# Kernel tuning notes

Measured on AMD Instinct MI355X. Metric: run time of the kernel, lower is better.

Reference implementation:

```python
import jax, jax.numpy as jnp
import numpy as np

CHEB_K = 3

def avwgcn(x, E, W_pool, b_pool):
    # x: [B,N,Cin], E: [N,e], W_pool: [e,K,Cin,Cout], b_pool: [e,Cout]
    N = E.shape[0]
    A = jax.nn.softmax(jax.nn.relu(E @ E.T), axis=1)          # adaptive adjacency [N,N]
    supports = [jnp.eye(N, dtype=x.dtype), A]
    for _ in range(2, CHEB_K):
        supports.append(2.0 * (A @ supports[-1]) - supports[-2])
    S = jnp.stack(supports)                                    # [K,N,N]
    W = jnp.einsum('ne,ekio->nkio', E, W_pool)                 # per-node weights
    b = E @ b_pool                                             # [N,Cout]
    xg = jnp.einsum('knm,bmi->bnki', S, x)                     # Chebyshev graph conv
    return jnp.einsum('bnki,nkio->bno', xg, W) + b


def setup_inputs() -> dict:
    key = jax.random.key(0)
    ks = jax.random.split(key, 7)
    B, N, Din, Dout, E_DIM = 64, 1024, 64, 64, 16
    C = Din + Dout
    return {
        'x': jax.random.normal(ks[0], (B, N, Din), dtype=jnp.float32),
        'state': jax.random.normal(ks[1], (B, N, Dout), dtype=jnp.float32),
        'node_embeddings': jax.random.normal(ks[2], (N, E_DIM), dtype=jnp.float32),
        'gate_W_pool': jax.random.normal(ks[3], (E_DIM, CHEB_K, C, 2 * Dout), dtype=jnp.float32) * 0.1,
        'gate_b_pool': jax.random.normal(ks[4], (E_DIM, 2 * Dout), dtype=jnp.float32) * 0.1,
        'upd_W_pool': jax.random.normal(ks[5], (E_DIM, CHEB_K, C, Dout), dtype=jnp.float32) * 0.1,
        'upd_b_pool': jax.random.normal(ks[6], (E_DIM, Dout), dtype=jnp.float32) * 0.1,
    }


def reference(x, state, node_embeddings, gate_W_pool, gate_b_pool, upd_W_pool, upd_b_pool):
    hidden_dim = state.shape[-1]
    input_and_state = jnp.concatenate([x, state], axis=-1)
    z_r = jax.nn.sigmoid(avwgcn(input_and_state, node_embeddings, gate_W_pool, gate_b_pool))
    z, r = z_r[..., :hidden_dim], z_r[..., hidden_dim:]
    candidate = jnp.concatenate([x, z * state], axis=-1)
    hc = jnp.tanh(avwgcn(candidate, node_embeddings, upd_W_pool, upd_b_pool))
    return r * state + (1.0 - r) * hc
```

## Files before the change

### kernel.cpp

```cpp
#include <hip/hip_runtime.h>
#include <math.h>

#define N_NODES 1024
#define B_SZ 64
#define GNH 4096
#define KI 384
#define EDIM 16

typedef _Float16 half8_t __attribute__((ext_vector_type(8)));
typedef float f32x4 __attribute__((ext_vector_type(4)));

__device__ __forceinline__ unsigned short f2h(float f) {
    _Float16 h = (_Float16)f;
    return *(unsigned short*)&h;
}
__device__ __forceinline__ float h2f(unsigned short u) {
    _Float16 h = *(_Float16*)&u;
    return (float)h;
}
__device__ __forceinline__ float sigmoidf_(float v) {
    return 1.f / (1.f + __expf(-v));
}
__device__ __forceinline__ void load_lds16(const void* g, void* l) {
    __builtin_amdgcn_global_load_lds(
        (const __attribute__((address_space(1))) void*)g,
        (__attribute__((address_space(3))) void*)l, 16, 0, 0);
}

__global__ __launch_bounds__(256) void compute_A_kernel(
    const float* __restrict__ E, unsigned short* __restrict__ Ah) {
    __shared__ float red[256];
    const int tid = threadIdx.x;
    const int n = blockIdx.x;
    float en[EDIM];
#pragma unroll
    for (int e = 0; e < EDIM; ++e) en[e] = E[n * EDIM + e];
    float logit[4], lmax = -1e30f;
#pragma unroll
    for (int j = 0; j < 4; ++j) {
        const int m = tid + j * 256;
        float d = 0.f;
#pragma unroll
        for (int e = 0; e < EDIM; ++e) d += en[e] * E[m * EDIM + e];
        d = fmaxf(d, 0.f);
        logit[j] = d;
        lmax = fmaxf(lmax, d);
    }
    red[tid] = lmax;
    __syncthreads();
    for (int s = 128; s > 0; s >>= 1) {
        if (tid < s) red[tid] = fmaxf(red[tid], red[tid + s]);
        __syncthreads();
    }
    lmax = red[0];
    __syncthreads();
    float ex[4], lsum = 0.f;
#pragma unroll
    for (int j = 0; j < 4; ++j) {
        ex[j] = __expf(logit[j] - lmax);
        lsum += ex[j];
    }
    red[tid] = lsum;
    __syncthreads();
    for (int s = 128; s > 0; s >>= 1) {
        if (tid < s) red[tid] += red[tid + s];
        __syncthreads();
    }
    const float inv = 1.f / red[0];
#pragma unroll
    for (int j = 0; j < 4; ++j)
        Ah[n * N_NODES + tid + j * 256] = f2h(ex[j] * inv);
}

__global__ __launch_bounds__(256) void build_T0_all_kernel(
    const float* __restrict__ x, const float* __restrict__ state,
    unsigned short* __restrict__ TX0, unsigned short* __restrict__ TS0,
    unsigned short* __restrict__ TX0T, unsigned short* __restrict__ TS0T) {
    __shared__ unsigned short Lx[64 * 72];
    __shared__ unsigned short Lss[64 * 72];
    const int tid = threadIdx.x;
    const int n0 = blockIdx.x * 64;
    const int b = blockIdx.y;
#pragma unroll
    for (int t = 0; t < 16; ++t) {
        const int id = t * 256 + tid;
        const int nl = id >> 6;
        const int c = id & 63;
        const float xv = x[((size_t)b * N_NODES + n0 + nl) * 64 + c];
        const float sv = state[((size_t)b * N_NODES + n0 + nl) * 64 + c];
        const unsigned short xh = f2h(xv), sh = f2h(sv);
        TX0[(size_t)(n0 + nl) * GNH + b * 64 + c] = xh;
        TS0[(size_t)(n0 + nl) * GNH + b * 64 + c] = sh;
        Lx[c * 72 + nl] = xh;
        Lss[c * 72 + nl] = sh;
    }
    __syncthreads();
#pragma unroll
    for (int t = 0; t < 2; ++t) {
        const int id = t * 256 + tid;
        const int c = id >> 3;
        const int n8 = id & 7;
        uint4 xv = *(const uint4*)&Lx[c * 72 + n8 * 8];
        uint4 sv = *(const uint4*)&Lss[c * 72 + n8 * 8];
        *(uint4*)&TX0T[(size_t)(b * 64 + c) * N_NODES + n0 + n8 * 8] = xv;
        *(uint4*)&TS0T[(size_t)(b * 64 + c) * N_NODES + n0 + n8 * 8] = sv;
    }
}

__global__ __launch_bounds__(256) void transpose16_kernel(
    const unsigned short* __restrict__ src, unsigned short* __restrict__ dst,
    int W) {
    __shared__ unsigned short Ls[64 * 72];
    const int tid = threadIdx.x;
    const int r0 = blockIdx.x * 64;
    const int c0 = blockIdx.y * 64;
#pragma unroll
    for (int t = 0; t < 2; ++t) {
        const int id = t * 256 + tid;
        const int row = id >> 3;
        const int c8 = id & 7;
        uint4 v = *(const uint4*)&src[(size_t)(r0 + row) * W + c0 + c8 * 8];
        const unsigned short* vp = (const unsigned short*)&v;
#pragma unroll
        for (int j = 0; j < 8; ++j) Ls[(c8 * 8 + j) * 72 + row] = vp[j];
    }
    __syncthreads();
#pragma unroll
    for (int t = 0; t < 2; ++t) {
        const int id = t * 256 + tid;
        const int c = id >> 3;
        const int r8 = id & 7;
        uint4 v = *(const uint4*)&Ls[c * 72 + r8 * 8];
        *(uint4*)&dst[(size_t)(c0 + c) * N_NODES + r0 + r8 * 8] = v;
    }
}

__global__ __launch_bounds__(256) void gemm_s2_kernel(
    const unsigned short* __restrict__ Ah,
    const unsigned short* __restrict__ AhT, unsigned short* __restrict__ S2h) {
    __shared__ unsigned short As[64 * 64];
    __shared__ unsigned short Bs[64 * 64];
    const int tid = threadIdx.x;
    const int wave = tid >> 6;
    const int lane = tid & 63;
    const int l15 = lane & 15;
    const int quad = lane >> 4;
    const int n0 = blockIdx.x * 64;
    const int m0 = blockIdx.y * 64;
    const int wn = wave * 16;
    const int lr = lane >> 3;
    const int lsw = (lane & 7) ^ lr;

    f32x4 acc[4] = {};
    for (int k0 = 0; k0 < N_NODES; k0 += 64) {
#pragma unroll
        for (int i = 0; i < 2; ++i) {
            const int rbase = (wave * 2 + i) * 8;
            load_lds16(&Ah[(size_t)(n0 + rbase + lr) * N_NODES + k0 + lsw * 8],
                       &As[rbase * 64]);
            load_lds16(&AhT[(size_t)(m0 + rbase + lr) * N_NODES + k0 + lsw * 8],
                       &Bs[rbase * 64]);
        }
        __syncthreads();
#pragma unroll
        for (int ks = 0; ks < 2; ++ks) {
            const int slot = ((ks * 4 + quad) ^ (l15 & 7)) * 8;
            const half8_t b = *(const half8_t*)&Bs[(wn + l15) * 64 + slot];
#pragma unroll
            for (int mi = 0; mi < 4; ++mi) {
                const half8_t a = *(const half8_t*)&As[(mi * 16 + l15) * 64 + slot];
                acc[mi] =
                    __builtin_amdgcn_mfma_f32_16x16x32_f16(a, b, acc[mi], 0, 0, 0);
            }
        }
        __syncthreads();
    }
#pragma unroll
    for (int mi = 0; mi < 4; ++mi) {
#pragma unroll
        for (int r = 0; r < 4; ++r) {
            const int n_g = n0 + mi * 16 + quad * 4 + r;
            const int m_g = m0 + wn + l15;
            const float v = 2.f * acc[mi][r] - (n_g == m_g ? 1.f : 0.f);
            S2h[(size_t)n_g * N_NODES + m_g] = f2h(v);
        }
    }
}

template <int BM>
__global__ __launch_bounds__(512, 2) void gemm_graph8_kernel(
    const unsigned short* __restrict__ Ah,
    const unsigned short* __restrict__ S2h,
    const unsigned short* __restrict__ BTX,
    const unsigned short* __restrict__ BTS,
    unsigned short* __restrict__ T1X, unsigned short* __restrict__ T1S,
    unsigned short* __restrict__ T2X, unsigned short* __restrict__ T2S,
    int ysplit, int colsPerXcd) {
    constexpr int MFR = BM / 32;
    constexpr int ASLOT_H = BM * 32;
    constexpr int SLOT_H = ASLOT_H + 8192;
    constexpr int APASS = BM / 128;
    constexpr int MT = 2048 / BM;
    __shared__ unsigned short lds[4 * SLOT_H];

    const int tid = threadIdx.x;
    const int wave = tid >> 6;
    const int lane = tid & 63;
    const int l15 = lane & 15;
    const int quad = lane >> 4;
    const int wm = (wave >> 2) * (BM / 2);
    const int wn = (wave & 3) * 64;

    const int id = blockIdx.x;
    const int xcd = id & 7;
    const int j = id >> 3;
    const int mtile = j & (MT - 1);
    const int ytile = xcd * colsPerXcd + j / MT;
    const int mrow0 = mtile * BM;
    const bool isA = mrow0 < N_NODES;
    const unsigned short* Asrc =
        (isA ? Ah : S2h) + (size_t)(mrow0 & 1023) * N_NODES;
    const bool isX = ytile < ysplit;
    const int col0 = (isX ? ytile : ytile - ysplit) * 256;
    const unsigned short* Bsrc = (isX ? BTX : BTS) + (size_t)col0 * N_NODES;
    unsigned short* OUT = (isA ? (isX ? T1X : T1S) : (isX ? T2X : T2S)) +
                          (size_t)(mrow0 & 1023) * GNH + col0;

    int goff[2];
#pragma unroll
    for (int jp = 0; jp < 2; ++jp) {
        const int cell = jp * 512 + tid;
        const int prow = cell >> 3;
        const int q = (cell & 7) ^ (prow & 7);
        goff[jp] = (2 * prow + (q >> 2)) * N_NODES + (q & 3) * 8;
    }

    int offA[MFR], offB[4];
#pragma unroll
    for (int mi = 0; mi < MFR; ++mi) {
        const int prow = (wm >> 1) + mi * 8 + (l15 >> 1);
        const int s8 = ((l15 & 1) * 4 + quad) ^ (prow & 7);
        offA[mi] = prow * 64 + s8 * 8;
    }
#pragma unroll
    for (int ni = 0; ni < 4; ++ni) {
        const int pcol = (wn >> 1) + ni * 8 + (l15 >> 1);
        const int s8 = ((l15 & 1) * 4 + quad) ^ (pcol & 7);
        offB[ni] = ASLOT_H + pcol * 64 + s8 * 8;
    }

    f32x4 acc[MFR][4] = {};

    auto stageA = [&](int t) {
        const int sl = t & 3;
#pragma unroll
        for (int jp = 0; jp < APASS; ++jp)
            load_lds16(Asrc + (size_t)t * 32 + goff[jp],
                       &lds[sl * SLOT_H + jp * 4096 + wave * 512]);
    };
    auto stageB = [&](int t) {
        const int sl = t & 3;
#pragma unroll
        for (int jp = 0; jp < 2; ++jp)
            load_lds16(Bsrc + (size_t)t * 32 + goff[jp],
                       &lds[sl * SLOT_H + ASLOT_H + jp * 4096 + wave * 512]);
    };
    auto waitPipe = [&] {
        if constexpr (BM == 256)
            asm volatile("s_waitcnt vmcnt(8)" ::: "memory");
        else
            asm volatile("s_waitcnt vmcnt(6)" ::: "memory");
    };

    auto tileBody = [&](int t, bool tail) {
        const unsigned short* base = &lds[(t & 3) * SLOT_H];
        half8_t a[MFR], b0, b1, b2, b3;
#pragma unroll
        for (int mi = 0; mi < MFR; ++mi)
            a[mi] = *(const half8_t*)&base[offA[mi]];
        b0 = *(const half8_t*)&base[offB[0]];
        b1 = *(const half8_t*)&base[offB[1]];
        if (!tail) stageA(t + 3);
        __builtin_amdgcn_sched_barrier(0);
        __builtin_amdgcn_s_barrier();
        asm volatile("s_waitcnt lgkmcnt(0)" ::: "memory");
        __builtin_amdgcn_sched_barrier(0);
        __builtin_amdgcn_s_setprio(1);
#pragma unroll
        for (int mi = 0; mi < MFR; ++mi) {
            acc[mi][0] = __builtin_amdgcn_mfma_f32_16x16x32_f16(
                a[mi], b0, acc[mi][0], 0, 0, 0);
            acc[mi][1] = __builtin_amdgcn_mfma_f32_16x16x32_f16(
                a[mi], b1, acc[mi][1], 0, 0, 0);
        }
        __builtin_amdgcn_s_setprio(0);
        __builtin_amdgcn_sched_barrier(0);
        __builtin_amdgcn_s_barrier();
        b2 = *(const half8_t*)&base[offB[2]];
        b3 = *(const half8_t*)&base[offB[3]];
        if (!tail) {
            stageB(t + 3);
            waitPipe();
        } else {
            asm volatile("s_waitcnt vmcnt(0)" ::: "memory");
        }
        __builtin_amdgcn_sched_barrier(0);
        __builtin_amdgcn_s_barrier();
        asm volatile("s_waitcnt lgkmcnt(0)" ::: "memory");
        __builtin_amdgcn_sched_barrier(0);
        __builtin_amdgcn_s_setprio(1);
#pragma unroll
        for (int mi = 0; mi < MFR; ++mi) {
            acc[mi][2] = __builtin_amdgcn_mfma_f32_16x16x32_f16(
                a[mi], b2, acc[mi][2], 0, 0, 0);
            acc[mi][3] = __builtin_amdgcn_mfma_f32_16x16x32_f16(
                a[mi], b3, acc[mi][3], 0, 0, 0);
        }
        __builtin_amdgcn_s_setprio(0);
        __builtin_amdgcn_sched_barrier(0);
        __builtin_amdgcn_s_barrier();
    };

    stageA(0); stageB(0);
    stageA(1); stageB(1);
    stageA(2); stageB(2);
    waitPipe();
    __builtin_amdgcn_s_barrier();
    __builtin_amdgcn_sched_barrier(0);

#pragma unroll 4
    for (int t = 0; t < 28; ++t) tileBody(t, false);
    tileBody(28, false);
    tileBody(29, true);
    tileBody(30, true);
    tileBody(31, true);

    constexpr int NPASS = BM / 64;
#pragma unroll
    for (int p = 0; p < NPASS; ++p) {
        __syncthreads();
        const int whalf = (BM == 256) ? (p >> 1) : p;
        const int mi0 = (BM == 256) ? (p & 1) * 4 : 0;
        if ((wave >> 2) == whalf) {
#pragma unroll
            for (int mi = 0; mi < 4; ++mi)
#pragma unroll
                for (int ni = 0; ni < 4; ++ni)
#pragma unroll
                    for (int r = 0; r < 4; ++r) {
                        const int row = mi * 16 + quad * 4 + r;
                        const int col = wn + ni * 16 + l15;
                        lds[row * 264 + col] = f2h(acc[mi0 + mi][ni][r]);
                    }
        }
        __syncthreads();
#pragma unroll
        for (int i = 0; i < 4; ++i) {
            const int id2 = i * 512 + tid;
            const int row = id2 >> 5;
            const int c8 = id2 & 31;
            uint4 v = *(const uint4*)&lds[row * 264 + c8 * 8];
            *(uint4*)&OUT[(size_t)(p * 64 + row) * GNH + c8 * 8] = v;
        }
    }
}

__global__ __launch_bounds__(256) void dequant_kernel(
    const float* __restrict__ Wp, const float* __restrict__ E,
    unsigned short* __restrict__ Wt, int NO) {
    __shared__ float En[32 * 16];
    const int tid = threadIdx.x;
    const int ki0 = blockIdx.x * 32;
    const int o0 = blockIdx.y * 32;
    const int n0 = blockIdx.z * 32;
    const int o = tid >> 3;
    const int k4 = tid & 7;

#pragma unroll
    for (int t = 0; t < 2; ++t) {
        const int id = t * 256 + tid;
        En[id] = E[(n0 + (id >> 4)) * EDIM + (id & 15)];
    }
    __syncthreads();

    f32x4 w[EDIM];
#pragma unroll
    for (int e = 0; e < EDIM; ++e) {
        f32x4 v;
#pragma unroll
        for (int j = 0; j < 4; ++j)
            v[j] = Wp[(size_t)(e * KI + ki0 + k4 * 4 + j) * NO + o0 + o];
        w[e] = v;
    }

    const size_t wt_base = ((size_t)n0 * NO + (o0 + o)) * KI + ki0 + k4 * 4;
#pragma unroll 4
    for (int nl = 0; nl < 32; ++nl) {
        f32x4 a = {0.f, 0.f, 0.f, 0.f};
#pragma unroll
        for (int e = 0; e < EDIM; ++e) a += w[e] * En[nl * EDIM + e];
        union { unsigned short u[4]; uint2 v; } pk;
#pragma unroll
        for (int j = 0; j < 4; ++j) pk.u[j] = f2h(a[j]);
        *(uint2*)&Wt[wt_base + (size_t)nl * NO * KI] = pk.v;
    }
}

__global__ __launch_bounds__(256) void pernode_gate_kernel(
    const unsigned short* __restrict__ TX0,
    const unsigned short* __restrict__ TS0,
    const unsigned short* __restrict__ TX1,
    const unsigned short* __restrict__ TS1,
    const unsigned short* __restrict__ TX2,
    const unsigned short* __restrict__ TS2,
    const unsigned short* __restrict__ Wt, const float* __restrict__ E,
    const float* __restrict__ bp, const float* __restrict__ state,
    unsigned short* __restrict__ rbuf, unsigned short* __restrict__ ts0_out) {
    __shared__ unsigned short XsX[64 * 64];
    __shared__ unsigned short XsS[64 * 64];
    const int n = blockIdx.x;
    const int tid = threadIdx.x;
    const int wave = tid >> 6;
    const int lane = tid & 63;
    const int l15 = lane & 15;
    const int quad = lane >> 4;
    const int wn = wave * 32;
    const int lr = lane >> 3;
    const int lsw = (lane & 7) ^ lr;

    float bias[2];
#pragma unroll
    for (int ni = 0; ni < 2; ++ni) {
        float bv = 0.f;
#pragma unroll
        for (int e = 0; e < EDIM; ++e)
            bv += E[n * EDIM + e] * bp[e * 128 + wn + ni * 16 + l15];
        bias[ni] = bv;
    }

    f32x4 acc[4][2] = {};

    const unsigned short* TXs[3] = {TX0, TX1, TX2};
    const unsigned short* TSs[3] = {TS0, TS1, TS2};
    const unsigned short* wrow0 = Wt + ((size_t)n * 128 + wn + l15) * KI;
    const unsigned short* wrow1 = Wt + ((size_t)n * 128 + wn + 16 + l15) * KI;

    for (int s = 0; s < 3; ++s) {
        const unsigned short* xs = TXs[s] + (size_t)n * GNH;
        const unsigned short* ss = TSs[s] + (size_t)n * GNH;
#pragma unroll
        for (int i = 0; i < 2; ++i) {
            const int slab = wave * 2 + i;
            load_lds16(xs + (slab * 8 + lr) * 64 + lsw * 8, &XsX[slab * 512]);
            load_lds16(ss + (slab * 8 + lr) * 64 + lsw * 8, &XsS[slab * 512]);
        }
        __syncthreads();
#pragma unroll
        for (int ks = 0; ks < 4; ++ks) {
            const int kseg = ks * 4 + quad;
            half8_t b[2];
            b[0] = *(const half8_t*)&wrow0[s * 128 + kseg * 8];
            b[1] = *(const half8_t*)&wrow1[s * 128 + kseg * 8];
            const unsigned short* plane = (kseg < 8) ? XsX : XsS;
            const int aslot = ((kseg & 7) ^ (l15 & 7)) * 8;
#pragma unroll
            for (int mi = 0; mi < 4; ++mi) {
                const half8_t a =
                    *(const half8_t*)&plane[(mi * 16 + l15) * 64 + aslot];
#pragma unroll
                for (int ni = 0; ni < 2; ++ni)
                    acc[mi][ni] = __builtin_amdgcn_mfma_f32_16x16x32_f16(
                        a, b[ni], acc[mi][ni], 0, 0, 0);
            }
        }
        __syncthreads();
    }

#pragma unroll
    for (int mi = 0; mi < 4; ++mi) {
#pragma unroll
        for (int r = 0; r < 4; ++r) {
            const int b_g = mi * 16 + quad * 4 + r;
#pragma unroll
            for (int ni = 0; ni < 2; ++ni) {
                const int o_g = wn + ni * 16 + l15;
                const float v = sigmoidf_(acc[mi][ni][r] + bias[ni]);
                if (o_g < 64) {
                    const float sv =
                        state[((size_t)b_g * N_NODES + n) * 64 + o_g];
                    ts0_out[(size_t)n * GNH + b_g * 64 + o_g] = f2h(v * sv);
                } else {
                    rbuf[((size_t)n * B_SZ + b_g) * 64 + (o_g - 64)] = f2h(v);
                }
            }
        }
    }
}

__global__ __launch_bounds__(256) void pernode_upd_kernel(
    const unsigned short* __restrict__ TX0,
    const unsigned short* __restrict__ TS0,
    const unsigned short* __restrict__ TX1,
    const unsigned short* __restrict__ TS1,
    const unsigned short* __restrict__ TX2,
    const unsigned short* __restrict__ TS2,
    const unsigned short* __restrict__ Wt, const float* __restrict__ E,
    const float* __restrict__ bp, const float* __restrict__ state,
    const unsigned short* __restrict__ rbuf, float* __restrict__ out) {
    __shared__ unsigned short XsX[64 * 64];
    __shared__ unsigned short XsS[64 * 64];
    const int n = blockIdx.x;
    const int tid = threadIdx.x;
    const int wave = tid >> 6;
    const int lane = tid & 63;
    const int l15 = lane & 15;
    const int quad = lane >> 4;
    const int wn = wave * 16;
    const int o_g = wn + l15;
    const int lr = lane >> 3;
    const int lsw = (lane & 7) ^ lr;

    float bias = 0.f;
#pragma unroll
    for (int e = 0; e < EDIM; ++e)
        bias += E[n * EDIM + e] * bp[e * 64 + o_g];

    f32x4 acc[4] = {};

    const unsigned short* TXs[3] = {TX0, TX1, TX2};
    const unsigned short* TSs[3] = {TS0, TS1, TS2};
    const unsigned short* wrow = Wt + ((size_t)n * 64 + o_g) * KI;

    for (int s = 0; s < 3; ++s) {
        const unsigned short* xs = TXs[s] + (size_t)n * GNH;
        const unsigned short* ss = TSs[s] + (size_t)n * GNH;
#pragma unroll
        for (int i = 0; i < 2; ++i) {
            const int slab = wave * 2 + i;
            load_lds16(xs + (slab * 8 + lr) * 64 + lsw * 8, &XsX[slab * 512]);
            load_lds16(ss + (slab * 8 + lr) * 64 + lsw * 8, &XsS[slab * 512]);
        }
        __syncthreads();
#pragma unroll
        for (int ks = 0; ks < 4; ++ks) {
            const int kseg = ks * 4 + quad;
            const half8_t b = *(const half8_t*)&wrow[s * 128 + kseg * 8];
            const unsigned short* plane = (kseg < 8) ? XsX : XsS;
            const int aslot = ((kseg & 7) ^ (l15 & 7)) * 8;
#pragma unroll
            for (int mi = 0; mi < 4; ++mi) {
                const half8_t a =
                    *(const half8_t*)&plane[(mi * 16 + l15) * 64 + aslot];
                acc[mi] = __builtin_amdgcn_mfma_f32_16x16x32_f16(a, b, acc[mi],
                                                                 0, 0, 0);
            }
        }
        __syncthreads();
    }

#pragma unroll
    for (int mi = 0; mi < 4; ++mi) {
#pragma unroll
        for (int r = 0; r < 4; ++r) {
            const int b_g = mi * 16 + quad * 4 + r;
            const float hc = tanhf(acc[mi][r] + bias);
            const float rr = h2f(rbuf[((size_t)n * B_SZ + b_g) * 64 + o_g]);
            const float sv = state[((size_t)b_g * N_NODES + n) * 64 + o_g];
            out[((size_t)b_g * N_NODES + n) * 64 + o_g] =
                rr * sv + (1.f - rr) * hc;
        }
    }
}

extern "C" void kernel_launch(void* const* d_in, const int* in_sizes, int n_in,
                              void* d_out, int out_size, void* d_ws,
                              size_t ws_size, hipStream_t stream) {
    const float* x = (const float*)d_in[0];
    const float* state = (const float*)d_in[1];
    const float* E = (const float*)d_in[2];
    const float* gW = (const float*)d_in[3];
    const float* gb = (const float*)d_in[4];
    const float* uW = (const float*)d_in[5];
    const float* ub = (const float*)d_in[6];
    float* out = (float*)d_out;

    char* ws = (char*)d_ws;
    unsigned short* Ah = (unsigned short*)ws;
    unsigned short* AhT = (unsigned short*)(ws + 2097152);
    unsigned short* S2h = (unsigned short*)(ws + 4194304);
    unsigned short* TX0 = (unsigned short*)(ws + 6291456);
    unsigned short* TS0 = (unsigned short*)(ws + 14680064);
    unsigned short* TX0T = (unsigned short*)(ws + 23068672);
    unsigned short* TS0T = (unsigned short*)(ws + 31457280);
    unsigned short* TX1 = (unsigned short*)(ws + 39845888);
    unsigned short* TS1 = (unsigned short*)(ws + 48234496);
    unsigned short* TX2 = (unsigned short*)(ws + 56623104);
    unsigned short* TS2 = (unsigned short*)(ws + 65011712);
    unsigned short* Wt = (unsigned short*)(ws + 73400320);
    unsigned short* rbuf = (unsigned short*)(ws + 174063616);

    compute_A_kernel<<<N_NODES, 256, 0, stream>>>(E, Ah);
    build_T0_all_kernel<<<dim3(16, 64), 256, 0, stream>>>(x, state, TX0, TS0,
                                                          TX0T, TS0T);
    transpose16_kernel<<<dim3(16, 16), 256, 0, stream>>>(Ah, AhT, N_NODES);
    gemm_s2_kernel<<<dim3(16, 16), 256, 0, stream>>>(Ah, AhT, S2h);

    gemm_graph8_kernel<256><<<256, 512, 0, stream>>>(
        Ah, S2h, TX0T, TS0T, TX1, TS1, TX2, TS2, 16, 4);
    dequant_kernel<<<dim3(12, 4, 32), 256, 0, stream>>>(gW, E, Wt, 128);
    pernode_gate_kernel<<<N_NODES, 256, 0, stream>>>(
        TX0, TS0, TX1, TS1, TX2, TS2, Wt, E, gb, state, rbuf, TS0);
    transpose16_kernel<<<dim3(16, 64), 256, 0, stream>>>(TS0, TS0T, GNH);

    gemm_graph8_kernel<128><<<256, 512, 0, stream>>>(
        Ah, S2h, TX0T, TS0T, TX1, TS1, TX2, TS2, 0, 2);
    dequant_kernel<<<dim3(12, 2, 32), 256, 0, stream>>>(uW, E, Wt, 64);
    pernode_upd_kernel<<<N_NODES, 256, 0, stream>>>(
        TX0, TS0, TX1, TS1, TX2, TS2, Wt, E, ub, state, rbuf, out);
}
```

Measured before the change: 293.2 us.

## Double-buffer LDS stages and preload weights in per-node gate/update kernels

The per-node gate and update kernels now load all weight fragments into registers up front. They double-buffer the three Chebyshev stages in LDS, issuing loads for the next stage while MFMAs run on the current one, with explicit vmcnt waits and barriers in place of the loop's syncthreads. The gate output now goes to a separate CAND buffer instead of overwriting TS0 in place, which avoids a write-after-read hazard now that stages are prefetched. The cost is more register pressure from the preloaded weights, twice the LDS, and hand-tuned wait counts that must match the issued loads.

Result: no change. 291.8 us (-0.5%).

```diff
diff --git a/kernel.cpp b/kernel.cpp
--- a/kernel.cpp
+++ b/kernel.cpp
@@ -25,6 +25,9 @@
     __builtin_amdgcn_global_load_lds(
         (const __attribute__((address_space(1))) void*)g,
         (__attribute__((address_space(3))) void*)l, 16, 0, 0);
+}
+__device__ __forceinline__ void fence_sched() {
+    __builtin_amdgcn_sched_barrier(0);
 }
 
 __global__ __launch_bounds__(256) void compute_A_kernel(
@@ -415,9 +418,8 @@
     const unsigned short* __restrict__ TS2,
     const unsigned short* __restrict__ Wt, const float* __restrict__ E,
     const float* __restrict__ bp, const float* __restrict__ state,
-    unsigned short* __restrict__ rbuf, unsigned short* __restrict__ ts0_out) {
-    __shared__ unsigned short XsX[64 * 64];
-    __shared__ unsigned short XsS[64 * 64];
+    unsigned short* __restrict__ rbuf, unsigned short* __restrict__ cand) {
+    __shared__ unsigned short Xs[2][2][4096];
     const int n = blockIdx.x;
     const int tid = threadIdx.x;
     const int wave = tid >> 6;
@@ -428,6 +430,16 @@
     const int lr = lane >> 3;
     const int lsw = (lane & 7) ^ lr;
 
+    const unsigned short* wrow0 = Wt + ((size_t)n * 128 + wn + l15) * KI;
+    const unsigned short* wrow1 = Wt + ((size_t)n * 128 + wn + 16 + l15) * KI;
+    half8_t wf[3][4][2];
+#pragma unroll
+    for (int s = 0; s < 3; ++s)
+#pragma unroll
+        for (int ks = 0; ks < 4; ++ks) {
+            wf[s][ks][0] = *(const half8_t*)&wrow0[s * 128 + (ks * 4 + quad) * 8];
+            wf[s][ks][1] = *(const half8_t*)&wrow1[s * 128 + (ks * 4 + quad) * 8];
+        }
     float bias[2];
 #pragma unroll
     for (int ni = 0; ni < 2; ++ni) {
@@ -438,30 +450,29 @@
         bias[ni] = bv;
     }
 
-    f32x4 acc[4][2] = {};
-
     const unsigned short* TXs[3] = {TX0, TX1, TX2};
     const unsigned short* TSs[3] = {TS0, TS1, TS2};
-    const unsigned short* wrow0 = Wt + ((size_t)n * 128 + wn + l15) * KI;
-    const unsigned short* wrow1 = Wt + ((size_t)n * 128 + wn + 16 + l15) * KI;
-
-    for (int s = 0; s < 3; ++s) {
+
+    auto STAGE = [&](int s, int bf) {
         const unsigned short* xs = TXs[s] + (size_t)n * GNH;
         const unsigned short* ss = TSs[s] + (size_t)n * GNH;
 #pragma unroll
         for (int i = 0; i < 2; ++i) {
             const int slab = wave * 2 + i;
-            load_lds16(xs + (slab * 8 + lr) * 64 + lsw * 8, &XsX[slab * 512]);
-            load_lds16(ss + (slab * 8 + lr) * 64 + lsw * 8, &XsS[slab * 512]);
-        }
-        __syncthreads();
+            load_lds16(xs + (slab * 8 + lr) * 64 + lsw * 8,
+                       &Xs[bf][0][slab * 512]);
+            load_lds16(ss + (slab * 8 + lr) * 64 + lsw * 8,
+                       &Xs[bf][1][slab * 512]);
+        }
+    };
+
+    f32x4 acc[4][2] = {};
+    auto MFMAS = [&](int s, int bf) {
 #pragma unroll
         for (int ks = 0; ks < 4; ++ks) {
             const int kseg = ks * 4 + quad;
-            half8_t b[2];
-            b[0] = *(const half8_t*)&wrow0[s * 128 + kseg * 8];
-            b[1] = *(const half8_t*)&wrow1[s * 128 + kseg * 8];
-            const unsigned short* plane = (kseg < 8) ? XsX : XsS;
+            const unsigned short* plane = (kseg < 8) ? &Xs[bf][0][0]
+                                                     : &Xs[bf][1][0];
             const int aslot = ((kseg & 7) ^ (l15 & 7)) * 8;
 #pragma unroll
             for (int mi = 0; mi < 4; ++mi) {
@@ -470,11 +481,34 @@
 #pragma unroll
                 for (int ni = 0; ni < 2; ++ni)
                     acc[mi][ni] = __builtin_amdgcn_mfma_f32_16x16x32_f16(
-                        a, b[ni], acc[mi][ni], 0, 0, 0);
+                        a, wf[s][ks][ni], acc[mi][ni], 0, 0, 0);
             }
         }
-        __syncthreads();
-    }
+    };
+
+    fence_sched();
+    asm volatile("s_waitcnt vmcnt(0)" ::: "memory");
+    fence_sched();
+    STAGE(0, 0);
+    STAGE(1, 1);
+    fence_sched();
+    asm volatile("s_waitcnt vmcnt(4)" ::: "memory");
+    fence_sched();
+    __builtin_amdgcn_s_barrier();
+    MFMAS(0, 0);
+    fence_sched();
+    __builtin_amdgcn_s_barrier();
+    STAGE(2, 0);
+    fence_sched();
+    asm volatile("s_waitcnt vmcnt(4)" ::: "memory");
+    fence_sched();
+    __builtin_amdgcn_s_barrier();
+    MFMAS(1, 1);
+    fence_sched();
+    asm volatile("s_waitcnt vmcnt(0)" ::: "memory");
+    fence_sched();
+    __builtin_amdgcn_s_barrier();
+    MFMAS(2, 0);
 
 #pragma unroll
     for (int mi = 0; mi < 4; ++mi) {
@@ -488,7 +522,7 @@
                 if (o_g < 64) {
                     const float sv =
                         state[((size_t)b_g * N_NODES + n) * 64 + o_g];
-                    ts0_out[(size_t)n * GNH + b_g * 64 + o_g] = f2h(v * sv);
+                    cand[(size_t)n * GNH + b_g * 64 + o_g] = f2h(v * sv);
                 } else {
                     rbuf[((size_t)n * B_SZ + b_g) * 64 + (o_g - 64)] = f2h(v);
                 }
@@ -499,7 +533,7 @@
 
 __global__ __launch_bounds__(256) void pernode_upd_kernel(
     const unsigned short* __restrict__ TX0,
-    const unsigned short* __restrict__ TS0,
+    const unsigned short* __restrict__ CAND,
     const unsigned short* __restrict__ TX1,
     const unsigned short* __restrict__ TS1,
     const unsigned short* __restrict__ TX2,
@@ -507,8 +541,7 @@
     const unsigned short* __restrict__ Wt, const float* __restrict__ E,
     const float* __restrict__ bp, const float* __restrict__ state,
     const unsigned short* __restrict__ rbuf, float* __restrict__ out) {
-    __shared__ unsigned short XsX[64 * 64];
-    __shared__ unsigned short XsS[64 * 64];
+    __shared__ unsigned short Xs[2][2][4096];
     const int n = blockIdx.x;
     const int tid = threadIdx.x;
     const int wave = tid >> 6;
@@ -520,43 +553,75 @@
     const int lr = lane >> 3;
     const int lsw = (lane & 7) ^ lr;
 
+    const unsigned short* wrow = Wt + ((size_t)n * 64 + o_g) * KI;
+    half8_t wf[3][4];
+#pragma unroll
+    for (int s = 0; s < 3; ++s)
+#pragma unroll
+        for (int ks = 0; ks < 4; ++ks)
+            wf[s][ks] = *(const half8_t*)&wrow[s * 128 + (ks * 4 + quad) * 8];
     float bias = 0.f;
 #pragma unroll
     for (int e = 0; e < EDIM; ++e)
         bias += E[n * EDIM + e] * bp[e * 64 + o_g];
 
-    f32x4 acc[4] = {};
-
     const unsigned short* TXs[3] = {TX0, TX1, TX2};
-    const unsigned short* TSs[3] = {TS0, TS1, TS2};
-    const unsigned short* wrow = Wt + ((size_t)n * 64 + o_g) * KI;
-
-    for (int s = 0; s < 3; ++s) {
+    const unsigned short* TSs[3] = {CAND, TS1, TS2};
+
+    auto STAGE = [&](int s, int bf) {
         const unsigned short* xs = TXs[s] + (size_t)n * GNH;
         const unsigned short* ss = TSs[s] + (size_t)n * GNH;
 #pragma unroll
         for (int i = 0; i < 2; ++i) {
             const int slab = wave * 2 + i;
-            load_lds16(xs + (slab * 8 + lr) * 64 + lsw * 8, &XsX[slab * 512]);
-            load_lds16(ss + (slab * 8 + lr) * 64 + lsw * 8, &XsS[slab * 512]);
-        }
-        __syncthreads();
+            load_lds16(xs + (slab * 8 + lr) * 64 + lsw * 8,
+                       &Xs[bf][0][slab * 512]);
+            load_lds16(ss + (slab * 8 + lr) * 64 + lsw * 8,
+                       &Xs[bf][1][slab * 512]);
+        }
+    };
+
+    f32x4 acc[4] = {};
+    auto MFMAS = [&](int s, int bf) {
 #pragma unroll
         for (int ks = 0; ks < 4; ++ks) {
             const int kseg = ks * 4 + quad;
-            const half8_t b = *(const half8_t*)&wrow[s * 128 + kseg * 8];
-            const unsigned short* plane = (kseg < 8) ? XsX : XsS;
+            const unsigned short* plane = (kseg < 8) ? &Xs[bf][0][0]
+                                                     : &Xs[bf][1][0];
             const int aslot = ((kseg & 7) ^ (l15 & 7)) * 8;
 #pragma unroll
             for (int mi = 0; mi < 4; ++mi) {
                 const half8_t a =
                     *(const half8_t*)&plane[(mi * 16 + l15) * 64 + aslot];
-                acc[mi] = __builtin_amdgcn_mfma_f32_16x16x32_f16(a, b, acc[mi],
-                                                                 0, 0, 0);
+                acc[mi] = __builtin_amdgcn_mfma_f32_16x16x32_f16(
+                    a, wf[s][ks], acc[mi], 0, 0, 0);
             }
         }
-        __syncthreads();
-    }
+    };
+
+    fence_sched();
+    asm volatile("s_waitcnt vmcnt(0)" ::: "memory");
+    fence_sched();
+    STAGE(0, 0);
+    STAGE(1, 1);
+    fence_sched();
+    asm volatile("s_waitcnt vmcnt(4)" ::: "memory");
+    fence_sched();
+    __builtin_amdgcn_s_barrier();
+    MFMAS(0, 0);
+    fence_sched();
+    __builtin_amdgcn_s_barrier();
+    STAGE(2, 0);
+    fence_sched();
+    asm volatile("s_waitcnt vmcnt(4)" ::: "memory");
+    fence_sched();
+    __builtin_amdgcn_s_barrier();
+    MFMAS(1, 1);
+    fence_sched();
+    asm volatile("s_waitcnt vmcnt(0)" ::: "memory");
+    fence_sched();
+    __builtin_amdgcn_s_barrier();
+    MFMAS(2, 0);
 
 #pragma unroll
     for (int mi = 0; mi < 4; ++mi) {
@@ -598,6 +663,7 @@
     unsigned short* TS2 = (unsigned short*)(ws + 65011712);
     unsigned short* Wt = (unsigned short*)(ws + 73400320);
     unsigned short* rbuf = (unsigned short*)(ws + 174063616);
+    unsigned short* CAND = (unsigned short*)(ws + 182452224);
 
     compute_A_kernel<<<N_NODES, 256, 0, stream>>>(E, Ah);
     build_T0_all_kernel<<<dim3(16, 64), 256, 0, stream>>>(x, state, TX0, TS0,
@@ -609,12 +675,12 @@
         Ah, S2h, TX0T, TS0T, TX1, TS1, TX2, TS2, 16, 4);
     dequant_kernel<<<dim3(12, 4, 32), 256, 0, stream>>>(gW, E, Wt, 128);
     pernode_gate_kernel<<<N_NODES, 256, 0, stream>>>(
-        TX0, TS0, TX1, TS1, TX2, TS2, Wt, E, gb, state, rbuf, TS0);
-    transpose16_kernel<<<dim3(16, 64), 256, 0, stream>>>(TS0, TS0T, GNH);
+        TX0, TS0, TX1, TS1, TX2, TS2, Wt, E, gb, state, rbuf, CAND);
+    transpose16_kernel<<<dim3(16, 64), 256, 0, stream>>>(CAND, TS0T, GNH);
 
     gemm_graph8_kernel<128><<<256, 512, 0, stream>>>(
         Ah, S2h, TX0T, TS0T, TX1, TS1, TX2, TS2, 0, 2);
     dequant_kernel<<<dim3(12, 2, 32), 256, 0, stream>>>(uW, E, Wt, 64);
     pernode_upd_kernel<<<N_NODES, 256, 0, stream>>>(
-        TX0, TS0, TX1, TS1, TX2, TS2, Wt, E, ub, state, rbuf, out);
-}
+        TX0, CAND, TX1, TS1, TX2, TS2, Wt, E, ub, state, rbuf, out);
+}
```
